# Optimization experiments

Measured on AMD Instinct MI355X. Metric: run time of the kernel, lower is better.

Reference implementation:

```python
import jax, jax.numpy as jnp
import numpy as np

B, D = 8192, 1024            # batch, inputs_dim
H1, H2, H3 = 2048, 1024, 512 # expert_units
NS, NT = 8, 4                # num_shared_experts, num_tasks_experts
E = NS + 3 * NT              # 20 experts total: [shared 0:8 | SA 8:12 | RA 12:16 | EA 16:20]
TU1, TU2 = 1024, 512         # tower_units
TIN = H3 * 4                 # tower input dim = 2048


def lrelu(x):
    return jnp.where(x >= 0, x, 0.1 * x)


def setup_inputs() -> dict:
    key = jax.random.key(0)
    ks = jax.random.split(key, 24)
    s = 0.02
    return {
        "inputs": jax.random.normal(ks[0], (B, D), jnp.float32),
        # stacked expert MLP params (leading axis = expert index)
        "W1": jax.random.normal(ks[1], (E, D, H1), jnp.float32) * s,
        "b1": jnp.zeros((E, H1), jnp.float32),
        "W2": jax.random.normal(ks[2], (E, H1, H2), jnp.float32) * s,
        "b2": jnp.zeros((E, H2), jnp.float32),
        "W3": jax.random.normal(ks[3], (E, H2, H3), jnp.float32) * s,
        "b3": jnp.zeros((E, H3), jnp.float32),
        # gate linears (single layer + softmax over dim 1)
        "Wg_sh": jax.random.normal(ks[4], (D, NS + 3 * NT), jnp.float32) * s,
        "bg_sh": jnp.zeros((NS + 3 * NT,), jnp.float32),
        "Wg_sa": jax.random.normal(ks[5], (D, NT + NS), jnp.float32) * s,
        "bg_sa": jnp.zeros((NT + NS,), jnp.float32),
        "Wg_ra": jax.random.normal(ks[6], (D, NT + NS), jnp.float32) * s,
        "bg_ra": jnp.zeros((NT + NS,), jnp.float32),
        "Wg_ea": jax.random.normal(ks[7], (D, NT + NS), jnp.float32) * s,
        "bg_ea": jnp.zeros((NT + NS,), jnp.float32),
        # 2 towers (one per task), stacked on leading axis
        "Wt1": jax.random.normal(ks[8], (2, TIN, TU1), jnp.float32) * s,
        "bt1": jnp.zeros((2, TU1), jnp.float32),
        "Wt2": jax.random.normal(ks[9], (2, TU1, TU2), jnp.float32) * s,
        "bt2": jnp.zeros((2, TU2), jnp.float32),
        # per-task output denses: PRESENCE=6, AIRFLOW=4
        "Wd0": jax.random.normal(ks[10], (TU2, 6), jnp.float32) * s,
        "bd0": jnp.zeros((6,), jnp.float32),
        "Wd1": jax.random.normal(ks[11], (TU2, 4), jnp.float32) * s,
        "bd1": jnp.zeros((4,), jnp.float32),
    }


def reference(inputs, W1, b1, W2, b2, W3, b3,
              Wg_sh, bg_sh, Wg_sa, bg_sa, Wg_ra, bg_ra, Wg_ea, bg_ea,
              Wt1, bt1, Wt2, bt2, Wd0, bd0, Wd1, bd1):
    x = inputs
    # all 20 experts as batched GEMMs: [E, B, h]
    h = lrelu(jnp.einsum('bd,edh->ebh', x, W1) + b1[:, None, :])
    h = lrelu(jnp.einsum('ebh,ehk->ebk', h, W2) + b2[:, None, :])
    eo = lrelu(jnp.einsum('ebk,eko->ebo', h, W3) + b3[:, None, :])  # [E,B,H3]

    # gates (softmax over feature dim)
    g_sh = jax.nn.softmax(x @ Wg_sh + bg_sh, axis=1)  # [B, 20]
    g_sa = jax.nn.softmax(x @ Wg_sa + bg_sa, axis=1)  # [B, 12]
    g_ra = jax.nn.softmax(x @ Wg_ra + bg_ra, axis=1)
    g_ea = jax.nn.softmax(x @ Wg_ea + bg_ea, axis=1)

    # shared gate: order = shared + SA + RA + EA == natural stacking order
    out_sh = jnp.einsum('ebh,be->bh', eo, g_sh)
    # task gates: order = task experts + shared experts
    out_sa = jnp.einsum('ebh,be->bh', jnp.concatenate([eo[NS:NS+NT], eo[:NS]], 0), g_sa)
    out_ra = jnp.einsum('ebh,be->bh', jnp.concatenate([eo[NS+NT:NS+2*NT], eo[:NS]], 0), g_ra)
    out_ea = jnp.einsum('ebh,be->bh', jnp.concatenate([eo[NS+2*NT:], eo[:NS]], 0), g_ea)

    tower_in = jnp.concatenate([out_sh, out_sa, out_ra, out_ea], axis=1)  # [B, 2048]
    t = lrelu(jnp.einsum('bi,kio->kbo', tower_in, Wt1) + bt1[:, None, :])  # [2,B,TU1]
    t = lrelu(jnp.einsum('kbo,kop->kbp', t, Wt2) + bt2[:, None, :])        # [2,B,TU2]
    out0 = t[0] @ Wd0 + bd0  # [B, 6]  PRESENCE
    out1 = t[1] @ Wd1 + bd1  # [B, 4]  AIRFLOW
    return (out0, out1)
```

## Files before the change

kernel.cpp:

```cpp
#include <hip/hip_runtime.h>

#define DEV __device__ __forceinline__

typedef __bf16 bf16x8 __attribute__((ext_vector_type(8)));
typedef float f32x4 __attribute__((ext_vector_type(4)));

DEV unsigned short f2bf(float f) {
  union { float f; unsigned u; } v; v.f = f;
  unsigned r = v.u + 0x7FFFu + ((v.u >> 16) & 1u);
  return (unsigned short)(r >> 16);
}
DEV float bf2f(unsigned short h) {
  union { float f; unsigned u; } v; v.u = ((unsigned)h) << 16;
  return v.f;
}

DEV void gload16(const void* g, void* l) {
  __builtin_amdgcn_global_load_lds(
      (__attribute__((address_space(1))) void*)(g),
      (__attribute__((address_space(3))) void*)(l), 16, 0, 0);
}

#define MFMA16(a, b, c) __builtin_amdgcn_mfma_f32_16x16x32_bf16((a), (b), (c), 0, 0, 0)

DEV void gemm256_body(
    const unsigned short* __restrict__ A,
    const unsigned short* __restrict__ Bt,
    const float* __restrict__ bias,
    unsigned short* __restrict__ Out,
    int K, int lda, int ldo, int nbx, int nby,
    long sA, long sB, long sBias, long sOut)
{
  int wg = blockIdx.x;
  {
    const int nwg = gridDim.x;
    const int q = nwg >> 3, r = nwg & 7;
    const int xcd = wg & 7, pos = wg >> 3;
    wg = (xcd < r ? xcd * (q + 1) : r * (q + 1) + (xcd - r) * q) + pos;
  }
  const int per_z = nbx * nby;
  const int z  = wg / per_z;
  const int rz = wg - z * per_z;
  const int by = rz / nbx;
  const int bx = rz - by * nbx;

  A    += (size_t)z * sA;
  Bt   += (size_t)z * sB;
  bias += (size_t)z * sBias;
  Out  += (size_t)z * sOut;

  const int tid  = threadIdx.x;
  const int lane = tid & 63;
  const int wid  = tid >> 6;
  const int wm   = wid >> 2, wn = wid & 3;
  const int m0   = by * 256, n0 = bx * 256;

  __shared__ alignas(16) char sm[2][65536];

  f32x4 acc[8][4];
  const f32x4 fz = {0.f, 0.f, 0.f, 0.f};
#pragma unroll
  for (int i = 0; i < 8; ++i)
#pragma unroll
    for (int j = 0; j < 4; ++j) acc[i][j] = fz;

  const int rr = tid >> 3;
  const int ch = (tid & 7) ^ (rr & 7);
  const char* gA = (const char*)A  + ((size_t)(m0 + rr) * lda) * 2 + ch * 16;
  const char* gB = (const char*)Bt + ((size_t)(n0 + rr) * K)   * 2 + ch * 16;
  const size_t stepA = (size_t)64 * lda * 2;
  const size_t stepB = (size_t)64 * K * 2;

  const int koff0 = (((lane >> 4) << 4) ^ ((lane & 7) << 4));
  const int aRow  = wm * 128 + (lane & 15);
  const int bRow  = wn * 64  + (lane & 15);

  const int nkt = K >> 6;

  auto SA = [&](int buf, int kt, int jh) {
    const char* s = gA + (size_t)kt * 128 + (2 * jh) * stepA;
    char* l = sm[buf] + tid * 16 + (2 * jh) * 8192;
    gload16(s, l);
    gload16(s + stepA, l + 8192);
  };
  auto SB = [&](int buf, int kt, int jh) {
    const char* s = gB + (size_t)kt * 128 + (2 * jh) * stepB;
    char* l = sm[buf] + 32768 + tid * 16 + (2 * jh) * 8192;
    gload16(s, l);
    gload16(s + stepB, l + 8192);
  };

  SA(0, 0, 0); SA(0, 0, 1); SB(0, 0, 0); SB(0, 0, 1);

  for (int kt = 0; kt < nkt; ++kt) {
    const int cur = kt & 1, nb = cur ^ 1;
    const bool pre = (kt + 1 < nkt);
    if (pre) {
      SA(nb, kt + 1, 0);
      asm volatile("s_waitcnt vmcnt(2)" ::: "memory");
    } else {
      asm volatile("s_waitcnt vmcnt(0)" ::: "memory");
    }
    __builtin_amdgcn_s_barrier();
    __builtin_amdgcn_sched_barrier(0);

    const char* pA = sm[cur] + aRow * 128;
    const char* pB = sm[cur] + 32768 + bRow * 128;
    bf16x8 a0[4], a1[4], b0[4], b1[4];

    {
#pragma unroll
      for (int i = 0; i < 4; ++i) a0[i] = *(const bf16x8*)(pA + i * 2048 + koff0);
#pragma unroll
      for (int n = 0; n < 4; ++n) b0[n] = *(const bf16x8*)(pB + n * 2048 + koff0);
      if (pre) SA(nb, kt + 1, 1);
      asm volatile("s_waitcnt lgkmcnt(0)" ::: "memory");
      __builtin_amdgcn_sched_barrier(0);
      __builtin_amdgcn_s_setprio(1);
#pragma unroll
      for (int i = 0; i < 4; ++i)
#pragma unroll
        for (int n = 0; n < 4; ++n) acc[i][n] = MFMA16(a0[i], b0[n], acc[i][n]);
      __builtin_amdgcn_s_setprio(0);
      __builtin_amdgcn_sched_barrier(0);
      __builtin_amdgcn_s_barrier();
      __builtin_amdgcn_sched_barrier(0);
    }
    {
#pragma unroll
      for (int i = 0; i < 4; ++i) a1[i] = *(const bf16x8*)(pA + (i + 4) * 2048 + koff0);
      if (pre) { SB(nb, kt + 1, 0); SB(nb, kt + 1, 1); }
      asm volatile("s_waitcnt lgkmcnt(0)" ::: "memory");
      __builtin_amdgcn_sched_barrier(0);
      __builtin_amdgcn_s_setprio(1);
#pragma unroll
      for (int i = 0; i < 4; ++i)
#pragma unroll
        for (int n = 0; n < 4; ++n) acc[i + 4][n] = MFMA16(a1[i], b0[n], acc[i + 4][n]);
      __builtin_amdgcn_s_setprio(0);
      __builtin_amdgcn_sched_barrier(0);
      __builtin_amdgcn_s_barrier();
      __builtin_amdgcn_sched_barrier(0);
    }
    {
      const int ko = koff0 ^ 64;
#pragma unroll
      for (int i = 0; i < 4; ++i) a0[i] = *(const bf16x8*)(pA + i * 2048 + ko);
#pragma unroll
      for (int n = 0; n < 4; ++n) b1[n] = *(const bf16x8*)(pB + n * 2048 + ko);
      asm volatile("s_waitcnt lgkmcnt(0)" ::: "memory");
      __builtin_amdgcn_sched_barrier(0);
      __builtin_amdgcn_s_setprio(1);
#pragma unroll
      for (int i = 0; i < 4; ++i)
#pragma unroll
        for (int n = 0; n < 4; ++n) acc[i][n] = MFMA16(a0[i], b1[n], acc[i][n]);
      __builtin_amdgcn_s_setprio(0);
      __builtin_amdgcn_sched_barrier(0);
      __builtin_amdgcn_s_barrier();
      __builtin_amdgcn_sched_barrier(0);
    }
    {
      const int ko = koff0 ^ 64;
#pragma unroll
      for (int i = 0; i < 4; ++i) a1[i] = *(const bf16x8*)(pA + (i + 4) * 2048 + ko);
      asm volatile("s_waitcnt lgkmcnt(0)" ::: "memory");
      __builtin_amdgcn_sched_barrier(0);
      __builtin_amdgcn_s_setprio(1);
#pragma unroll
      for (int i = 0; i < 4; ++i)
#pragma unroll
        for (int n = 0; n < 4; ++n) acc[i + 4][n] = MFMA16(a1[i], b1[n], acc[i + 4][n]);
      __builtin_amdgcn_s_setprio(0);
      __builtin_amdgcn_sched_barrier(0);
      __builtin_amdgcn_s_barrier();
      __builtin_amdgcn_sched_barrier(0);
    }
  }

#pragma unroll
  for (int ni = 0; ni < 4; ++ni) {
    const int c = n0 + wn * 64 + ni * 16 + (lane & 15);
    const float bv = bias[c];
#pragma unroll
    for (int mi = 0; mi < 8; ++mi) {
      const int r0 = m0 + wm * 128 + mi * 16 + ((lane >> 4) << 2);
#pragma unroll
      for (int j = 0; j < 4; ++j) {
        float v = acc[mi][ni][j] + bv;
        v = v >= 0.f ? v : 0.1f * v;
        Out[(size_t)(r0 + j) * ldo + c] = f2bf(v);
      }
    }
  }
}

#define GEMM_DEF(NAME)                                                        \
__global__ __launch_bounds__(512) void NAME(                                  \
    const unsigned short* __restrict__ A,                                     \
    const unsigned short* __restrict__ Bt,                                    \
    const float* __restrict__ bias,                                           \
    unsigned short* __restrict__ Out,                                         \
    int K, int lda, int ldo, int nbx, int nby,                                \
    long sA, long sB, long sBias, long sOut) {                                \
  gemm256_body(A, Bt, bias, Out, K, lda, ldo, nbx, nby, sA, sB, sBias, sOut); \
}
GEMM_DEF(gemm_l1)
GEMM_DEF(gemm_l2)
GEMM_DEF(gemm_l3)
GEMM_DEF(gemm_tw)

DEV float gateW(const float* Wsh, const float* Wsa, const float* Wra,
                const float* Wea, int k, int c) {
  if (c < 20) return Wsh[(size_t)k * 20 + c];
  if (c < 32) return Wsa[(size_t)k * 12 + (c - 20)];
  if (c < 44) return Wra[(size_t)k * 12 + (c - 32)];
  if (c < 56) return Wea[(size_t)k * 12 + (c - 44)];
  return 0.f;
}
DEV float gateB(const float* bsh, const float* bsa, const float* bra,
                const float* bea, int c) {
  if (c < 20) return bsh[c];
  if (c < 32) return bsa[c - 20];
  if (c < 44) return bra[c - 32];
  if (c < 56) return bea[c - 44];
  return 0.f;
}

__global__ __launch_bounds__(256) void prep_all(
    const float* __restrict__ W1,  const float* __restrict__ W2,
    const float* __restrict__ W3,  const float* __restrict__ Wt1,
    const float* __restrict__ Wt2, const float* __restrict__ x,
    const float* __restrict__ Wsh, const float* __restrict__ bsh,
    const float* __restrict__ Wsa, const float* __restrict__ bsa,
    const float* __restrict__ Wra, const float* __restrict__ bra,
    const float* __restrict__ Wea, const float* __restrict__ bea,
    unsigned short* __restrict__ W1t,  unsigned short* __restrict__ W2t,
    unsigned short* __restrict__ W3t,  unsigned short* __restrict__ Wt1t,
    unsigned short* __restrict__ Wt2t, unsigned short* __restrict__ xb,
    float* __restrict__ logits)
{
  const int id = blockIdx.x;
  const int t  = threadIdx.x;

  if (id < 128) {
    __shared__ alignas(16) float smg[4096];
    float (*sx)[64] = (float (*)[64])smg;
    float (*sw)[64] = (float (*)[64])(smg + 2048);
    const int b0 = id * 64;
    const int tr = t >> 4, tc = t & 15;
    float acc[4][4] = {};

    for (int kt = 0; kt < 32; ++kt) {
      const int k0 = kt * 32;
      __syncthreads();
#pragma unroll
      for (int it = 0; it < 2; ++it) {
        const int idx = t + it * 256;
        const int r = idx >> 3, c4 = (idx & 7) * 4;
        const float4 v = *(const float4*)(x + (size_t)(b0 + r) * 1024 + k0 + c4);
        sx[c4 + 0][r] = v.x; sx[c4 + 1][r] = v.y;
        sx[c4 + 2][r] = v.z; sx[c4 + 3][r] = v.w;
      }
#pragma unroll
      for (int it = 0; it < 2; ++it) {
        const int idx = t + it * 256;
        const int row = idx >> 4;
        const int c4  = (idx & 15) * 4;
#pragma unroll
        for (int j = 0; j < 4; ++j)
          sw[row][c4 + j] = gateW(Wsh, Wsa, Wra, Wea, k0 + row, c4 + j);
      }
      __syncthreads();
#pragma unroll
      for (int kk = 0; kk < 32; ++kk) {
        const float4 rx = *(const float4*)&sx[kk][tr * 4];
        const float4 wv = *(const float4*)&sw[kk][tc * 4];
#pragma unroll
        for (int i = 0; i < 4; ++i) {
          const float xv = (i == 0) ? rx.x : (i == 1) ? rx.y : (i == 2) ? rx.z : rx.w;
          acc[i][0] += xv * wv.x; acc[i][1] += xv * wv.y;
          acc[i][2] += xv * wv.z; acc[i][3] += xv * wv.w;
        }
      }
    }
    float bv[4];
#pragma unroll
    for (int j = 0; j < 4; ++j) bv[j] = gateB(bsh, bsa, bra, bea, tc * 4 + j);
#pragma unroll
    for (int i = 0; i < 4; ++i) {
      float4 o;
      o.x = acc[i][0] + bv[0]; o.y = acc[i][1] + bv[1];
      o.z = acc[i][2] + bv[2]; o.w = acc[i][3] + bv[3];
      *(float4*)&logits[(size_t)(b0 + tr * 4 + i) * 64 + tc * 4] = o;
    }
    return;
  }

  if (id >= 24448) {
    const int local = id - 24448;
    const int r0 = (local >> 4) * 64, c0 = (local & 15) * 64;
#pragma unroll
    for (int i = 0; i < 4; ++i) {
      const int row = r0 + i * 16 + (t >> 4);
      const int col = c0 + (t & 15) * 4;
      const float4 v = *(const float4*)(x + (size_t)row * 1024 + col);
      ushort4 u = make_ushort4(f2bf(v.x), f2bf(v.y), f2bf(v.z), f2bf(v.w));
      *(ushort4*)(xb + (size_t)row * 1024 + col) = u;
    }
    return;
  }

  const int g = id - 128;
  const float* src; unsigned short* dst; int K, N, local;
  if (g < 10240)      { src = W1;  dst = W1t;  K = 1024; N = 2048; local = g; }
  else if (g < 20480) { src = W2;  dst = W2t;  K = 2048; N = 1024; local = g - 10240; }
  else if (g < 23040) { src = W3;  dst = W3t;  K = 1024; N = 512;  local = g - 20480; }
  else if (g < 24064) { src = Wt1; dst = Wt1t; K = 2048; N = 1024; local = g - 23040; }
  else                { src = Wt2; dst = Wt2t; K = 1024; N = 512;  local = g - 24064; }

  const int nkt = K >> 6, nnt = N >> 6;
  const int per_z = nkt * nnt;
  const int z   = local / per_z;
  const int rem = local - z * per_z;
  const int k0  = (rem % nkt) * 64;
  const int n0  = (rem / nkt) * 64;
  src += (size_t)z * K * N;
  dst += (size_t)z * K * N;

  const int i4 = (t >> 4) * 4;
  const int j4 = (t & 15) * 4;
  float a[4][4];
#pragma unroll
  for (int rr = 0; rr < 4; ++rr)
    *(float4*)a[rr] = *(const float4*)(src + (size_t)(k0 + i4 + rr) * N + n0 + j4);
#pragma unroll
  for (int c = 0; c < 4; ++c) {
    ushort4 u = make_ushort4(f2bf(a[0][c]), f2bf(a[1][c]),
                             f2bf(a[2][c]), f2bf(a[3][c]));
    *(ushort4*)(dst + (size_t)(n0 + j4 + c) * K + k0 + i4) = u;
  }
}

__global__ __launch_bounds__(256) void combine_k(
    const unsigned short* __restrict__ eo,
    const float* __restrict__ logits,
    unsigned short* __restrict__ tin)
{
  const int b = blockIdx.x;
  const int t = threadIdx.x;
  __shared__ alignas(16) unsigned short lds[20][512];
  __shared__ float gsm[56];
  const unsigned short* er = eo + (size_t)b * 10240;
  unsigned short* ldsf = &lds[0][0];
#pragma unroll
  for (int i = 0; i < 5; ++i)
    gload16(er + (i * 256 + t) * 8, ldsf + (i * 256 + t) * 8);

  if (t < 64) {
    const float v0 = (t < 56) ? logits[(size_t)b * 64 + t] : 0.f;
    const int off[4] = {0, 20, 32, 44};
    const int wd[4]  = {20, 12, 12, 12};
    for (int g = 0; g < 4; ++g) {
      const bool in = (t >= off[g]) && (t < off[g] + wd[g]);
      float vv = in ? v0 : -1e30f;
      float m = vv;
#pragma unroll
      for (int o = 32; o; o >>= 1) m = fmaxf(m, __shfl_xor(m, o));
      float e = in ? __expf(vv - m) : 0.f;
      float s = e;
#pragma unroll
      for (int o = 32; o; o >>= 1) s += __shfl_xor(s, o);
      if (in) gsm[t] = e / s;
    }
  }
  __syncthreads();

  const int sec = t >> 6;
  const int h0 = (t & 63) * 8;
  float acc[8] = {0.f, 0.f, 0.f, 0.f, 0.f, 0.f, 0.f, 0.f};
  if (sec == 0) {
    for (int e = 0; e < 20; ++e) {
      const float w = gsm[e];
#pragma unroll
      for (int j = 0; j < 8; ++j) acc[j] += w * bf2f(lds[e][h0 + j]);
    }
  } else {
    const int goff = 20 + (sec - 1) * 12;
    const int ebase = 8 + (sec - 1) * 4;
    for (int tt = 0; tt < 4; ++tt) {
      const float w = gsm[goff + tt];
#pragma unroll
      for (int j = 0; j < 8; ++j) acc[j] += w * bf2f(lds[ebase + tt][h0 + j]);
    }
    for (int ss = 0; ss < 8; ++ss) {
      const float w = gsm[goff + 4 + ss];
#pragma unroll
      for (int j = 0; j < 8; ++j) acc[j] += w * bf2f(lds[ss][h0 + j]);
    }
  }
  unsigned short* ob = tin + (size_t)b * 2048 + sec * 512 + h0;
  ushort4 u0 = make_ushort4(f2bf(acc[0]), f2bf(acc[1]), f2bf(acc[2]), f2bf(acc[3]));
  ushort4 u1 = make_ushort4(f2bf(acc[4]), f2bf(acc[5]), f2bf(acc[6]), f2bf(acc[7]));
  *(ushort4*)ob = u0;
  *(ushort4*)(ob + 4) = u1;
}

__global__ __launch_bounds__(256) void outd_k(
    const unsigned short* __restrict__ t2,
    const float* __restrict__ Wd0, const float* __restrict__ bd0,
    const float* __restrict__ Wd1, const float* __restrict__ bd1,
    float* __restrict__ out)
{
  const int gid = blockIdx.x * 4 + (threadIdx.x >> 6);
  const int lane = threadIdx.x & 63;
  const int b = gid >> 1, task = gid & 1;
  const uint4 raw = *(const uint4*)(t2 + ((size_t)task * 8192 + b) * 512 + lane * 8);
  const unsigned short* rs = (const unsigned short*)&raw;
  float v[8];
#pragma unroll
  for (int j = 0; j < 8; ++j) v[j] = bf2f(rs[j]);
  const float* Wd = task ? Wd1 : Wd0;
  const float* bd = task ? bd1 : bd0;
  const int ncol = task ? 4 : 6;
  float* ob = task ? (out + (size_t)8192 * 6 + (size_t)b * 4) : (out + (size_t)b * 6);
  for (int c = 0; c < ncol; ++c) {
    float p = 0.f;
#pragma unroll
    for (int j = 0; j < 8; ++j) p += v[j] * Wd[(size_t)(lane * 8 + j) * ncol + c];
#pragma unroll
    for (int o = 32; o; o >>= 1) p += __shfl_xor(p, o);
    if (lane == 0) ob[c] = p + bd[c];
  }
}

extern "C" void kernel_launch(void* const* d_in, const int* in_sizes, int n_in,
                              void* d_out, int out_size, void* d_ws, size_t ws_size,
                              hipStream_t stream) {
  const float* x     = (const float*)d_in[0];
  const float* W1    = (const float*)d_in[1];
  const float* b1    = (const float*)d_in[2];
  const float* W2    = (const float*)d_in[3];
  const float* b2    = (const float*)d_in[4];
  const float* W3    = (const float*)d_in[5];
  const float* b3    = (const float*)d_in[6];
  const float* Wg_sh = (const float*)d_in[7];
  const float* bg_sh = (const float*)d_in[8];
  const float* Wg_sa = (const float*)d_in[9];
  const float* bg_sa = (const float*)d_in[10];
  const float* Wg_ra = (const float*)d_in[11];
  const float* bg_ra = (const float*)d_in[12];
  const float* Wg_ea = (const float*)d_in[13];
  const float* bg_ea = (const float*)d_in[14];
  const float* Wt1   = (const float*)d_in[15];
  const float* bt1   = (const float*)d_in[16];
  const float* Wt2   = (const float*)d_in[17];
  const float* bt2   = (const float*)d_in[18];
  const float* Wd0   = (const float*)d_in[19];
  const float* bd0   = (const float*)d_in[20];
  const float* Wd1   = (const float*)d_in[21];
  const float* bd1   = (const float*)d_in[22];
  float* out = (float*)d_out;

  const int B = 8192, D = 1024, H1 = 2048, H2 = 1024, H3 = 512;
  const int E = 20, TU1 = 1024, TU2 = 512, TIN = 2048;

  auto rnd = [](size_t n) { return (n + 255) & ~(size_t)255; };
  const size_t szTin  = rnd((size_t)B * TIN * 2);
  const size_t szT1   = rnd((size_t)2 * B * TU1 * 2);
  const size_t szT2   = rnd((size_t)2 * B * TU2 * 2);
  const size_t szH1e  = rnd((size_t)B * H1 * 2);
  const size_t szH2e  = rnd((size_t)B * H2 * 2);
  const size_t fixed = rnd((size_t)B * D * 2) + rnd((size_t)E * H1 * D * 2) +
                       rnd((size_t)E * H2 * H1 * 2) + rnd((size_t)E * H3 * H2 * 2) +
                       rnd((size_t)2 * TU1 * TIN * 2) + rnd((size_t)2 * TU2 * TU1 * 2) +
                       rnd((size_t)B * 64 * 4) + rnd((size_t)E * B * H3 * 2);
  const size_t tNeed = szTin + szT1 + szT2;

  const int G = 2;
  int hg = 2;
  {
    const int opts[3] = {10, 5, 2};
    for (int i = 0; i < 3; ++i) {
      size_t hNeed = (size_t)G * szH1e + (size_t)opts[i] * szH2e;
      if (hNeed < tNeed) hNeed = tNeed;
      if (fixed + hNeed <= ws_size) { hg = opts[i]; break; }
    }
  }

  char* w = (char*)d_ws;
  auto alloc = [&](size_t n) { char* p = w; w += rnd(n); return p; };
  unsigned short* xb   = (unsigned short*)alloc((size_t)B * D * 2);
  unsigned short* W1t  = (unsigned short*)alloc((size_t)E * H1 * D * 2);
  unsigned short* W2t  = (unsigned short*)alloc((size_t)E * H2 * H1 * 2);
  unsigned short* W3t  = (unsigned short*)alloc((size_t)E * H3 * H2 * 2);
  unsigned short* Wt1t = (unsigned short*)alloc((size_t)2 * TU1 * TIN * 2);
  unsigned short* Wt2t = (unsigned short*)alloc((size_t)2 * TU2 * TU1 * 2);
  float*          lgts = (float*)alloc((size_t)B * 64 * 4);
  unsigned short* eo   = (unsigned short*)alloc((size_t)E * B * H3 * 2);
  char* hreg = w;
  unsigned short* h1  = (unsigned short*)hreg;
  unsigned short* h2  = (unsigned short*)(hreg + (size_t)G * szH1e);
  unsigned short* tin = (unsigned short*)hreg;
  unsigned short* t1  = (unsigned short*)(hreg + szTin);
  unsigned short* t2  = (unsigned short*)(hreg + szTin + szT1);
  (void)in_sizes; (void)n_in; (void)out_size;

  prep_all<<<dim3(26496), 256, 0, stream>>>(
      W1, W2, W3, Wt1, Wt2, x,
      Wg_sh, bg_sh, Wg_sa, bg_sa, Wg_ra, bg_ra, Wg_ea, bg_ea,
      W1t, W2t, W3t, Wt1t, Wt2t, xb, lgts);

  for (int e0 = 0; e0 < E; e0 += G) {
    gemm_l1<<<dim3((H1 / 256) * (B / 256) * G), 512, 0, stream>>>(
        xb, W1t + (size_t)e0 * H1 * D, b1 + (size_t)e0 * H1, h1,
        D, D, H1, H1 / 256, B / 256, 0, (long)H1 * D, (long)H1, (long)B * H1);
    gemm_l2<<<dim3((H2 / 256) * (B / 256) * G), 512, 0, stream>>>(
        h1, W2t + (size_t)e0 * H2 * H1, b2 + (size_t)e0 * H2,
        h2 + (size_t)(e0 % hg) * B * H2,
        H1, H1, H2, H2 / 256, B / 256,
        (long)B * H1, (long)H2 * H1, (long)H2, (long)B * H2);
    if ((e0 + G) % hg == 0) {
      const int eb = e0 + G - hg;
      gemm_l3<<<dim3((H3 / 256) * (B / 256) * hg), 512, 0, stream>>>(
          h2, W3t + (size_t)eb * H3 * H2, b3 + (size_t)eb * H3,
          eo + (size_t)eb * H3,
          H2, H2, E * H3, H3 / 256, B / 256,
          (long)B * H2, (long)H3 * H2, (long)H3, (long)H3);
    }
  }

  combine_k<<<dim3(B), 256, 0, stream>>>(eo, lgts, tin);

  gemm_tw<<<dim3((TU1 / 256) * (B / 256) * 2), 512, 0, stream>>>(
      tin, Wt1t, bt1, t1, TIN, TIN, TU1, TU1 / 256, B / 256,
      0, (long)TU1 * TIN, (long)TU1, (long)B * TU1);
  gemm_tw<<<dim3((TU2 / 256) * (B / 256) * 2), 512, 0, stream>>>(
      t1, Wt2t, bt2, t2, TU1, TU1, TU2, TU2 / 256, B / 256,
      (long)B * TU1, (long)TU2 * TU1, (long)TU2, (long)B * TU2);

  outd_k<<<dim3(B * 2 / 4), 256, 0, stream>>>(t2, Wd0, bd0, Wd1, bd1, out);
}
```

Measured before the change: 2.116 ms.

## Overlap layer-1 and layer-2 expert GEMMs in one dual-GEMM launch

Adds a `gemm_dual` kernel that splits its grid between two independent GEMM problems. The host loop is software-pipelined so each launch runs layer 1 for expert pair k alongside layer 2 for pair k-1. Layer-1 outputs are double-buffered and layer 3 runs every four experts. The aim is to fill idle compute units and cut kernel launches and tail effects, but it drops the workspace-size check and relies on a fixed buffer footprint.

```diff
diff --git a/kernel.cpp b/kernel.cpp
--- a/kernel.cpp
+++ b/kernel.cpp
@@ -29,11 +29,11 @@
     const float* __restrict__ bias,
     unsigned short* __restrict__ Out,
     int K, int lda, int ldo, int nbx, int nby,
-    long sA, long sB, long sBias, long sOut)
+    long sA, long sB, long sBias, long sOut,
+    int bid, int nwg)
 {
-  int wg = blockIdx.x;
+  int wg = bid;
   {
-    const int nwg = gridDim.x;
     const int q = nwg >> 3, r = nwg & 7;
     const int xcd = wg & 7, pos = wg >> 3;
     wg = (xcd < r ? xcd * (q + 1) : r * (q + 1) + (xcd - r) * q) + pos;
@@ -195,6 +195,35 @@
   }
 }
 
+__global__ __launch_bounds__(512) void gemm_dual(
+    const unsigned short* A1, const unsigned short* Bt1, const float* bias1,
+    unsigned short* O1, int K1, int lda1, int ldo1, int nbx1, int nby1,
+    long sA1, long sB1, long sBias1, long sO1,
+    const unsigned short* A2, const unsigned short* Bt2, const float* bias2,
+    unsigned short* O2, int K2, int lda2, int ldo2, int nbx2, int nby2,
+    long sA2, long sB2, long sBias2, long sO2,
+    int split)
+{
+  const bool one = ((int)blockIdx.x < split);
+  const unsigned short* A  = one ? A1 : A2;
+  const unsigned short* Bt = one ? Bt1 : Bt2;
+  const float* bias        = one ? bias1 : bias2;
+  unsigned short* Out      = one ? O1 : O2;
+  const int K   = one ? K1 : K2;
+  const int lda = one ? lda1 : lda2;
+  const int ldo = one ? ldo1 : ldo2;
+  const int nbx = one ? nbx1 : nbx2;
+  const int nby = one ? nby1 : nby2;
+  const long sA = one ? sA1 : sA2;
+  const long sB = one ? sB1 : sB2;
+  const long sBias = one ? sBias1 : sBias2;
+  const long sOut  = one ? sO1 : sO2;
+  const int bid = one ? (int)blockIdx.x : (int)blockIdx.x - split;
+  const int nwg = one ? split : (int)gridDim.x - split;
+  gemm256_body(A, Bt, bias, Out, K, lda, ldo, nbx, nby, sA, sB, sBias, sOut,
+               bid, nwg);
+}
+
 #define GEMM_DEF(NAME)                                                        \
 __global__ __launch_bounds__(512) void NAME(                                  \
     const unsigned short* __restrict__ A,                                     \
@@ -203,10 +232,9 @@
     unsigned short* __restrict__ Out,                                         \
     int K, int lda, int ldo, int nbx, int nby,                                \
     long sA, long sB, long sBias, long sOut) {                                \
-  gemm256_body(A, Bt, bias, Out, K, lda, ldo, nbx, nby, sA, sB, sBias, sOut); \
-}
-GEMM_DEF(gemm_l1)
-GEMM_DEF(gemm_l2)
+  gemm256_body(A, Bt, bias, Out, K, lda, ldo, nbx, nby, sA, sB, sBias, sOut,  \
+               (int)blockIdx.x, (int)gridDim.x);                              \
+}
 GEMM_DEF(gemm_l3)
 GEMM_DEF(gemm_tw)
 
@@ -466,27 +494,10 @@
   const int E = 20, TU1 = 1024, TU2 = 512, TIN = 2048;
 
   auto rnd = [](size_t n) { return (n + 255) & ~(size_t)255; };
-  const size_t szTin  = rnd((size_t)B * TIN * 2);
-  const size_t szT1   = rnd((size_t)2 * B * TU1 * 2);
-  const size_t szT2   = rnd((size_t)2 * B * TU2 * 2);
-  const size_t szH1e  = rnd((size_t)B * H1 * 2);
-  const size_t szH2e  = rnd((size_t)B * H2 * 2);
-  const size_t fixed = rnd((size_t)B * D * 2) + rnd((size_t)E * H1 * D * 2) +
-                       rnd((size_t)E * H2 * H1 * 2) + rnd((size_t)E * H3 * H2 * 2) +
-                       rnd((size_t)2 * TU1 * TIN * 2) + rnd((size_t)2 * TU2 * TU1 * 2) +
-                       rnd((size_t)B * 64 * 4) + rnd((size_t)E * B * H3 * 2);
-  const size_t tNeed = szTin + szT1 + szT2;
-
-  const int G = 2;
-  int hg = 2;
-  {
-    const int opts[3] = {10, 5, 2};
-    for (int i = 0; i < 3; ++i) {
-      size_t hNeed = (size_t)G * szH1e + (size_t)opts[i] * szH2e;
-      if (hNeed < tNeed) hNeed = tNeed;
-      if (fixed + hNeed <= ws_size) { hg = opts[i]; break; }
-    }
-  }
+  const size_t szTin = rnd((size_t)B * TIN * 2);
+  const size_t szT1  = rnd((size_t)2 * B * TU1 * 2);
+  const size_t szH1e = rnd((size_t)B * H1 * 2);
+  const size_t szH2e = rnd((size_t)B * H2 * 2);
 
   char* w = (char*)d_ws;
   auto alloc = [&](size_t n) { char* p = w; w += rnd(n); return p; };
@@ -500,31 +511,41 @@
   unsigned short* eo   = (unsigned short*)alloc((size_t)E * B * H3 * 2);
   char* hreg = w;
   unsigned short* h1  = (unsigned short*)hreg;
-  unsigned short* h2  = (unsigned short*)(hreg + (size_t)G * szH1e);
+  unsigned short* h2  = (unsigned short*)(hreg + 4 * szH1e);
   unsigned short* tin = (unsigned short*)hreg;
   unsigned short* t1  = (unsigned short*)(hreg + szTin);
   unsigned short* t2  = (unsigned short*)(hreg + szTin + szT1);
-  (void)in_sizes; (void)n_in; (void)out_size;
+  (void)in_sizes; (void)n_in; (void)out_size; (void)ws_size;
 
   prep_all<<<dim3(26496), 256, 0, stream>>>(
       W1, W2, W3, Wt1, Wt2, x,
       Wg_sh, bg_sh, Wg_sa, bg_sa, Wg_ra, bg_ra, Wg_ea, bg_ea,
       W1t, W2t, W3t, Wt1t, Wt2t, xb, lgts);
 
-  for (int e0 = 0; e0 < E; e0 += G) {
-    gemm_l1<<<dim3((H1 / 256) * (B / 256) * G), 512, 0, stream>>>(
-        xb, W1t + (size_t)e0 * H1 * D, b1 + (size_t)e0 * H1, h1,
-        D, D, H1, H1 / 256, B / 256, 0, (long)H1 * D, (long)H1, (long)B * H1);
-    gemm_l2<<<dim3((H2 / 256) * (B / 256) * G), 512, 0, stream>>>(
-        h1, W2t + (size_t)e0 * H2 * H1, b2 + (size_t)e0 * H2,
-        h2 + (size_t)(e0 % hg) * B * H2,
-        H1, H1, H2, H2 / 256, B / 256,
-        (long)B * H1, (long)H2 * H1, (long)H2, (long)B * H2);
-    if ((e0 + G) % hg == 0) {
-      const int eb = e0 + G - hg;
-      gemm_l3<<<dim3((H3 / 256) * (B / 256) * hg), 512, 0, stream>>>(
-          h2, W3t + (size_t)eb * H3 * H2, b3 + (size_t)eb * H3,
-          eo + (size_t)eb * H3,
+  for (int k = 0; k <= 10; ++k) {
+    const bool has1 = (k < 10), has2 = (k > 0);
+    const int split = has1 ? 512 : 0;
+    const int total = split + (has2 ? 256 : 0);
+    const int p1 = k, p2 = k - 1;
+    const unsigned short* A1 = xb;
+    const unsigned short* B1 = W1t + (size_t)(2 * (has1 ? p1 : 0)) * H1 * D;
+    const float* bb1 = b1 + (size_t)(2 * (has1 ? p1 : 0)) * H1;
+    unsigned short* O1 = h1 + (size_t)((has1 ? p1 : 0) & 1) * 2 * B * H1;
+    const unsigned short* A2 = h1 + (size_t)((has2 ? p2 : 0) & 1) * 2 * B * H1;
+    const unsigned short* B2 = W2t + (size_t)(2 * (has2 ? p2 : 0)) * H2 * H1;
+    const float* bb2 = b2 + (size_t)(2 * (has2 ? p2 : 0)) * H2;
+    unsigned short* O2 = h2 + (size_t)((2 * (has2 ? p2 : 0)) & 3) * B * H2;
+    gemm_dual<<<dim3(total), 512, 0, stream>>>(
+        A1, B1, bb1, O1, D, D, H1, H1 / 256, B / 256,
+        0, (long)H1 * D, (long)H1, (long)B * H1,
+        A2, B2, bb2, O2, H1, H1, H2, H2 / 256, B / 256,
+        (long)B * H1, (long)H2 * H1, (long)H2, (long)B * H2,
+        split);
+    if (k >= 2 && (k & 1) == 0) {
+      const int w2 = (k - 2) / 2;
+      gemm_l3<<<dim3((H3 / 256) * (B / 256) * 4), 512, 0, stream>>>(
+          h2, W3t + (size_t)(4 * w2) * H3 * H2, b3 + (size_t)(4 * w2) * H3,
+          eo + (size_t)(4 * w2) * H3,
           H2, H2, E * H3, H3 / 256, B / 256,
           (long)B * H2, (long)H3 * H2, (long)H3, (long)H3);
     }
```

Result: faster. 2.064 ms (-2.4%).
